# Kernel tuning notes

Hardware: AMD Instinct MI355X
Metric: run time of the kernel (lower is better)

The kernel has to match this reference:

```python
import jax, jax.numpy as jnp
import numpy as np


def setup_inputs() -> dict:
    key = jax.random.key(0)
    k1, k2, k3, k4 = jax.random.split(key, 4)
    B, C, H, W = 4, 512, 64, 64
    K = 20
    Cp = C // 4  # 128, proj_feat output channels
    feat = jax.random.normal(k1, (B, C, H, W), dtype=jnp.float32)
    cam = jax.random.uniform(k2, (B, K, H, W), dtype=jnp.float32)
    # 1x1 conv == linear over channel dim; store kernel as [Cout, Cin]
    w_proj = jax.random.normal(k3, (Cp, C), dtype=jnp.float32) * (1.0 / np.sqrt(C))
    b_proj = jax.random.normal(k4, (Cp,), dtype=jnp.float32) * 0.01
    return {"feat": feat, "cam": cam, "w_proj": w_proj, "b_proj": b_proj}


def reference(feat, cam, w_proj, b_proj):
    B, C, H, W = feat.shape
    K = cam.shape[1]
    N = H * W
    cam_detach = jax.lax.stop_gradient(cam)
    # proj_feat: 1x1 conv -> [B, N, C//4] token layout (matches view+transpose)
    feat_proj = jnp.einsum('bchw,oc->bhwo', feat, w_proj) + b_proj
    feat_proj = feat_proj.reshape(B, N, -1)                      # [B, N, Cp]
    cam_reshape = cam_detach.reshape(B, K, N)                    # [B, K, N]
    class_term = jnp.einsum('bkn,bnd->bkd', cam_reshape, feat_proj)  # [B, K, Cp]
    # unscaled self-attention over N pixels
    pixel_sim = jnp.einsum('bnd,bmd->bnm', feat_proj, feat_proj)     # [B, N, N]
    pixel_sim = jax.nn.softmax(pixel_sim, axis=-1)
    pixel_term = jnp.einsum('bnm,bmd->bnd', pixel_sim, feat_proj)    # [B, N, Cp]
    aug_cam = jnp.einsum('bkd,bnd->bkn', class_term, pixel_term)     # [B, K, N]
    return cam + aug_cam.reshape(B, K, H, W)
```

## Files before the change

kernel.cpp:

```cpp
#include <hip/hip_runtime.h>
#include <hip/hip_bf16.h>
#include <math.h>

#define NB 4
#define NC 512
#define NN 4096
#define NK 20
#define NCP 128
#define SPLIT 4
#define CHUNK (NN / SPLIT)
#define NTILES (CHUNK / 64)

typedef __bf16 bf16x8 __attribute__((ext_vector_type(8)));
typedef float f32x4 __attribute__((ext_vector_type(4)));
typedef float f32x16 __attribute__((ext_vector_type(16)));
typedef short short8 __attribute__((ext_vector_type(8)));
typedef unsigned int uint4v __attribute__((ext_vector_type(4)));

static __device__ __forceinline__ unsigned short f2bf(float f) {
    unsigned int u = __builtin_bit_cast(unsigned int, f);
    unsigned int r = (u + 0x7FFFu + ((u >> 16) & 1u)) >> 16;
    return (unsigned short)r;
}
static __device__ __forceinline__ float bf2f(unsigned short h) {
    unsigned int u = ((unsigned int)h) << 16;
    return __builtin_bit_cast(float, u);
}
static __device__ __forceinline__ bf16x8 ldbf8(const unsigned short* p) {
    return __builtin_bit_cast(bf16x8, *reinterpret_cast<const short8*>(p));
}
static __device__ __forceinline__ void gld16(const unsigned short* g, unsigned short* l) {
    __builtin_amdgcn_global_load_lds(
        (const __attribute__((address_space(1))) unsigned int*)g,
        (__attribute__((address_space(3))) unsigned int*)l, 16, 0, 0);
}
static __device__ __forceinline__ unsigned int cvtpk(float lo, float hi) {
    unsigned int r;
    asm("v_cvt_pk_bf16_f32 %0, %1, %2" : "=v"(r) : "v"(lo), "v"(hi));
    return r;
}

#define MFMA16(a, b, c) __builtin_amdgcn_mfma_f32_16x16x32_bf16(a, b, c, 0, 0, 0)
#define MFMA32(a, b, c) __builtin_amdgcn_mfma_f32_32x32x16_bf16(a, b, c, 0, 0, 0)
#define SCHED0() __builtin_amdgcn_sched_barrier(0)
#define BAR() do { SCHED0(); __builtin_amdgcn_s_barrier(); SCHED0(); } while (0)

__global__ __launch_bounds__(256) void wconv_kernel(
    const float* __restrict__ w, unsigned short* __restrict__ wb)
{
    int i = blockIdx.x * 256 + threadIdx.x;
    float4 v = reinterpret_cast<const float4*>(w)[i];
    unsigned int lo = (unsigned int)f2bf(v.x) | ((unsigned int)f2bf(v.y) << 16);
    unsigned int hi = (unsigned int)f2bf(v.z) | ((unsigned int)f2bf(v.w) << 16);
    reinterpret_cast<uint2*>(wb)[i] = make_uint2(lo, hi);
}

__global__ __launch_bounds__(256) void proj_kernel(
    const float* __restrict__ feat, const unsigned short* __restrict__ wb,
    const float* __restrict__ bias, unsigned short* __restrict__ fp,
    unsigned short* __restrict__ fpT)
{
    const int b = blockIdx.y;
    const int n0 = blockIdx.x * 64;
    const int tid = threadIdx.x;
    const int wid = tid >> 6;
    const int lane = tid & 63;
    const int lg = lane >> 4, lr = lane & 15;

    __shared__ unsigned short lds_f[2][64][40];

    const float* featb = feat + (size_t)b * NC * NN;

    f32x4 acc[2][4];
    #pragma unroll
    for (int i = 0; i < 2; ++i)
        #pragma unroll
        for (int j = 0; j < 4; ++j) acc[i][j] = (f32x4){0.f, 0.f, 0.f, 0.f};

    float4 pre[2];
    #pragma unroll
    for (int it = 0; it < 2; ++it) {
        int idx = it * 256 + tid;
        int cc = idx >> 4, q = idx & 15;
        pre[it] = *reinterpret_cast<const float4*>(&featb[(size_t)cc * NN + n0 + q * 4]);
    }

    for (int c0 = 0; c0 < NC; c0 += 32) {
        const int cur = (c0 >> 5) & 1;
        #pragma unroll
        for (int it = 0; it < 2; ++it) {
            int idx = it * 256 + tid;
            int cc = idx >> 4, q = idx & 15;
            float4 v = pre[it];
            lds_f[cur][q * 4 + 0][cc] = f2bf(v.x);
            lds_f[cur][q * 4 + 1][cc] = f2bf(v.y);
            lds_f[cur][q * 4 + 2][cc] = f2bf(v.z);
            lds_f[cur][q * 4 + 3][cc] = f2bf(v.w);
        }
        __syncthreads();
        if (c0 + 32 < NC) {
            #pragma unroll
            for (int it = 0; it < 2; ++it) {
                int idx = it * 256 + tid;
                int cc = idx >> 4, q = idx & 15;
                pre[it] = *reinterpret_cast<const float4*>(
                    &featb[(size_t)(c0 + 32 + cc) * NN + n0 + q * 4]);
            }
        }
        bf16x8 afr[2];
        #pragma unroll
        for (int dt = 0; dt < 2; ++dt)
            afr[dt] = ldbf8(&wb[(size_t)(wid * 32 + dt * 16 + lr) * NC + c0 + lg * 8]);
        #pragma unroll
        for (int n1 = 0; n1 < 4; ++n1) {
            bf16x8 bfr = ldbf8(&lds_f[cur][n1 * 16 + lr][lg * 8]);
            #pragma unroll
            for (int dt = 0; dt < 2; ++dt)
                acc[dt][n1] = MFMA16(afr[dt], bfr, acc[dt][n1]);
        }
    }
    #pragma unroll
    for (int dt = 0; dt < 2; ++dt)
        #pragma unroll
        for (int n1 = 0; n1 < 4; ++n1)
            #pragma unroll
            for (int i = 0; i < 4; ++i) {
                int d = wid * 32 + dt * 16 + lg * 4 + i;
                int n = n0 + n1 * 16 + lr;
                unsigned short h = f2bf(acc[dt][n1][i] + bias[d]);
                fp[((size_t)b * NN + n) * NCP + d] = h;
                fpT[((size_t)b * NCP + d) * NN + n] = h;
            }
}

__global__ __launch_bounds__(128) void ct_kernel(
    const float* __restrict__ cam, const unsigned short* __restrict__ fp,
    float* __restrict__ ct)
{
    const int bid = blockIdx.x;
    const int chunk = bid & 15;
    const int bk = bid >> 4;
    const int b = bk / NK, k = bk % NK;
    const int d2 = threadIdx.x & 63;
    const int half = threadIdx.x >> 6;
    const int nbase = chunk * 256 + half * 128;
    const float* camp = cam + ((size_t)b * NK + k) * NN + nbase;
    const unsigned short* fpp = fp + ((size_t)b * NN + nbase) * NCP + d2 * 2;
    float ax = 0.f, ay = 0.f;
    #pragma unroll 8
    for (int n = 0; n < 128; ++n) {
        float c = camp[n];
        unsigned int v = *reinterpret_cast<const unsigned int*>(&fpp[(size_t)n * NCP]);
        ax += c * bf2f((unsigned short)(v & 0xffff));
        ay += c * bf2f((unsigned short)(v >> 16));
    }
    float* ctp = &ct[((size_t)b * NK + k) * NCP + d2 * 2];
    atomicAdd(ctp, ax);
    atomicAdd(ctp + 1, ay);
}

__global__ __launch_bounds__(256, 3) void attn_partial_kernel(
    const unsigned short* __restrict__ fp, const unsigned short* __restrict__ fpT,
    unsigned short* __restrict__ po, float* __restrict__ mbuf, float* __restrict__ lbuf)
{
    const int b = blockIdx.z;
    const int sidx = blockIdx.y;
    const int tid = threadIdx.x;
    const int wid = tid >> 6;
    const int lane = tid & 63;
    const int l31 = lane & 31, hi = lane >> 5;
    const int q0 = blockIdx.x * 128 + wid * 32;
    const int kvbase = sidx * CHUNK;

    __shared__ unsigned short kt[2][64 * 128];
    __shared__ unsigned short vt[64 * 128];

    const unsigned short* fpb  = fp  + (size_t)b * NN * NCP;
    const unsigned short* fpTb = fpT + (size_t)b * NCP * NN;

    int offK[4], offV[4];
    #pragma unroll
    for (int i = 0; i < 4; ++i) {
        int oc = i * 256 + tid;
        int rk = oc >> 4, ck = oc & 15;
        offK[i] = rk * NCP + ((ck ^ (rk & 15)) << 3);
        int rowp = oc >> 4, cv = oc & 15;
        int cg = cv ^ (rowp & 15);
        int d = rowp * 2 + (cg >> 3), kvc = cg & 7;
        offV[i] = d * NN + (kvc << 3);
    }

    bf16x8 qf[8];
    #pragma unroll
    for (int kk = 0; kk < 8; ++kk)
        qf[kk] = ldbf8(&fpb[(size_t)(q0 + l31) * NCP + kk * 16 + hi * 8]);

    f32x16 o[4];
    #pragma unroll
    for (int dt = 0; dt < 4; ++dt)
        #pragma unroll
        for (int j = 0; j < 16; ++j) o[dt][j] = 0.f;
    float m_i = -INFINITY, l_i = 0.f;

    {
        const unsigned short* k0 = fpb + (size_t)kvbase * NCP;
        #pragma unroll
        for (int i = 0; i < 4; ++i)
            gld16(k0 + offK[i], &kt[0][(i * 256 + wid * 64) * 8]);
    }
    SCHED0();
    asm volatile("s_waitcnt vmcnt(0)" ::: "memory");
    BAR();

    for (int t = 0; t < NTILES; ++t) {
        const int cur = t & 1;
        {
            const unsigned short* vnow = fpTb + kvbase + t * 64;
            #pragma unroll
            for (int i = 0; i < 4; ++i)
                gld16(vnow + offV[i], &vt[(i * 256 + wid * 64) * 8]);
            const int tn = (t + 1) & (NTILES - 1);
            const unsigned short* knext = fpb + (size_t)(kvbase + tn * 64) * NCP;
            #pragma unroll
            for (int i = 0; i < 4; ++i)
                gld16(knext + offK[i], &kt[cur ^ 1][(i * 256 + wid * 64) * 8]);
        }
        SCHED0();
        const unsigned short* ktc = &kt[cur][0];
        f32x16 s[2];
        #pragma unroll
        for (int g = 0; g < 2; ++g)
            #pragma unroll
            for (int j = 0; j < 16; ++j) s[g][j] = 0.f;
        __builtin_amdgcn_s_setprio(1);
        #pragma unroll
        for (int kk = 0; kk < 8; ++kk) {
            #pragma unroll
            for (int g = 0; g < 2; ++g) {
                int row = g * 32 + l31;
                bf16x8 kf = ldbf8(&ktc[row * 128 + (((kk * 2 + hi) ^ (row & 15)) << 3)]);
                s[g] = MFMA32(kf, qf[kk], s[g]);
            }
        }
        __builtin_amdgcn_s_setprio(0);
        float pmax = s[0][0];
        #pragma unroll
        for (int g = 0; g < 2; ++g)
            #pragma unroll
            for (int j = 0; j < 16; ++j) pmax = fmaxf(pmax, s[g][j]);
        pmax = fmaxf(pmax, __shfl_xor(pmax, 32));
        if (!__all(pmax - m_i <= 8.f)) {
            float mnew = fmaxf(m_i, pmax);
            float sc = __expf(m_i - mnew);
            l_i *= sc;
            #pragma unroll
            for (int dt = 0; dt < 4; ++dt)
                #pragma unroll
                for (int j = 0; j < 16; ++j) o[dt][j] *= sc;
            m_i = mnew;
        }
        float sum = 0.f;
        #pragma unroll
        for (int g = 0; g < 2; ++g)
            #pragma unroll
            for (int j = 0; j < 16; ++j) {
                float e = __expf(s[g][j] - m_i);
                s[g][j] = e;
                sum += e;
            }
        sum += __shfl_xor(sum, 32);
        l_i += sum;
        unsigned int wk[2][8];
        #pragma unroll
        for (int g = 0; g < 2; ++g)
            #pragma unroll
            for (int m = 0; m < 8; ++m)
                wk[g][m] = cvtpk(s[g][2 * m], s[g][2 * m + 1]);
        bf16x8 pf[4];
        #pragma unroll
        for (int g = 0; g < 2; ++g)
            #pragma unroll
            for (int sub = 0; sub < 2; ++sub) {
                unsigned int A0 = wk[g][4 * sub],     B0 = wk[g][4 * sub + 2];
                unsigned int A1 = wk[g][4 * sub + 1], B1 = wk[g][4 * sub + 3];
                asm("v_permlane32_swap_b32 %0, %1" : "+v"(A0), "+v"(B0));
                asm("v_permlane32_swap_b32 %0, %1" : "+v"(A1), "+v"(B1));
                uint4v u;
                u[0] = A0; u[1] = A1; u[2] = B0; u[3] = B1;
                pf[2 * g + sub] = __builtin_bit_cast(bf16x8, u);
            }
        SCHED0();
        asm volatile("s_waitcnt vmcnt(4)" ::: "memory");
        BAR();
        __builtin_amdgcn_s_setprio(1);
        #pragma unroll
        for (int c2 = 0; c2 < 4; ++c2) {
            #pragma unroll
            for (int dt = 0; dt < 4; ++dt) {
                int row32 = dt * 32 + l31;
                int rowp = row32 >> 1;
                int chunk = (row32 & 1) * 8 + c2 * 2 + hi;
                bf16x8 vf = ldbf8(&vt[rowp * 128 + ((chunk ^ (rowp & 15)) << 3)]);
                o[dt] = MFMA32(vf, pf[c2], o[dt]);
            }
        }
        __builtin_amdgcn_s_setprio(0);
        SCHED0();
        asm volatile("s_waitcnt vmcnt(0)" ::: "memory");
        BAR();
    }
    const size_t pbase = (size_t)(b * SPLIT + sidx) * NN + q0;
    const size_t rowoff = (pbase + l31) * NCP;
    #pragma unroll
    for (int dt = 0; dt < 4; ++dt)
        #pragma unroll
        for (int qd = 0; qd < 4; ++qd) {
            unsigned int u0 = cvtpk(o[dt][qd * 4 + 0], o[dt][qd * 4 + 1]);
            unsigned int u1 = cvtpk(o[dt][qd * 4 + 2], o[dt][qd * 4 + 3]);
            *reinterpret_cast<uint2*>(&po[rowoff + dt * 32 + qd * 8 + hi * 4]) =
                make_uint2(u0, u1);
        }
    if (hi == 0) {
        mbuf[pbase + l31] = m_i;
        lbuf[pbase + l31] = l_i;
    }
}

__global__ __launch_bounds__(256) void aug_kernel(
    const float* __restrict__ cam, const float* __restrict__ ct,
    const unsigned short* __restrict__ po, const float* __restrict__ mbuf,
    const float* __restrict__ lbuf, float* __restrict__ out)
{
    const int b = blockIdx.y;
    const int tid = threadIdx.x, wid = tid >> 6, lane = tid & 63;
    const int lg = lane >> 4, lr = lane & 15;
    const int n0 = blockIdx.x * 64 + wid * 16;
    const int row = n0 + lr;
    const float* ctb = ct + (size_t)b * NK * NCP;

    float m_s[SPLIT], l_s[SPLIT], M = -INFINITY;
    #pragma unroll
    for (int s = 0; s < SPLIT; ++s) {
        m_s[s] = mbuf[(size_t)(b * SPLIT + s) * NN + row];
        l_s[s] = lbuf[(size_t)(b * SPLIT + s) * NN + row];
        M = fmaxf(M, m_s[s]);
    }
    float L = 0.f, wgt[SPLIT];
    #pragma unroll
    for (int s = 0; s < SPLIT; ++s) { wgt[s] = __expf(m_s[s] - M); L += wgt[s] * l_s[s]; }
    const float inv = 1.f / L;
    #pragma unroll
    for (int s = 0; s < SPLIT; ++s) wgt[s] *= inv;

    f32x4 acc[2];
    acc[0] = (f32x4){0.f, 0.f, 0.f, 0.f};
    acc[1] = (f32x4){0.f, 0.f, 0.f, 0.f};
    #pragma unroll
    for (int kk = 0; kk < 4; ++kk) {
        float mg[8];
        #pragma unroll
        for (int j = 0; j < 8; ++j) mg[j] = 0.f;
        #pragma unroll
        for (int s = 0; s < SPLIT; ++s) {
            uint4v v = *reinterpret_cast<const uint4v*>(
                &po[((size_t)(b * SPLIT + s) * NN + row) * NCP + kk * 32 + lg * 8]);
            #pragma unroll
            for (int j = 0; j < 4; ++j) {
                mg[2 * j]     += wgt[s] * bf2f((unsigned short)(v[j] & 0xffff));
                mg[2 * j + 1] += wgt[s] * bf2f((unsigned short)(v[j] >> 16));
            }
        }
        uint4v au;
        #pragma unroll
        for (int j = 0; j < 4; ++j) au[j] = cvtpk(mg[2 * j], mg[2 * j + 1]);
        bf16x8 af = __builtin_bit_cast(bf16x8, au);
        #pragma unroll
        for (int c = 0; c < 2; ++c) {
            int k = c * 16 + lr;
            short8 bv;
            if (k < NK) {
                const float* cr = &ctb[(size_t)k * NCP + kk * 32 + lg * 8];
                #pragma unroll
                for (int j = 0; j < 8; ++j) bv[j] = (short)f2bf(cr[j]);
            } else {
                #pragma unroll
                for (int j = 0; j < 8; ++j) bv[j] = 0;
            }
            acc[c] = MFMA16(af, __builtin_bit_cast(bf16x8, bv), acc[c]);
        }
    }
    #pragma unroll
    for (int c = 0; c < 2; ++c) {
        int k = c * 16 + lr;
        if (k < NK) {
            #pragma unroll
            for (int i = 0; i < 4; ++i) {
                size_t off = ((size_t)b * NK + k) * NN + n0 + lg * 4 + i;
                out[off] = cam[off] + acc[c][i];
            }
        }
    }
}

extern "C" void kernel_launch(void* const* d_in, const int* in_sizes, int n_in,
                              void* d_out, int out_size, void* d_ws, size_t ws_size,
                              hipStream_t stream) {
    const float* feat = (const float*)d_in[0];
    const float* cam  = (const float*)d_in[1];
    const float* wpr  = (const float*)d_in[2];
    const float* bpr  = (const float*)d_in[3];
    float* out = (float*)d_out;

    const size_t MB = 1024 * 1024;
    char* ws = (char*)d_ws;
    unsigned short* fp  = (unsigned short*)(ws);
    unsigned short* fpT = (unsigned short*)(ws + 4 * MB);
    float* ct           = (float*)(ws + 12 * MB);
    unsigned short* wb  = (unsigned short*)(ws + 12 * MB + 512 * 1024);
    unsigned short* po  = (unsigned short*)(ws + 13 * MB);
    float* mbuf         = (float*)(ws + 30 * MB);
    float* lbuf         = (float*)(ws + 31 * MB);

    hipMemsetAsync(ct, 0, (size_t)NB * NK * NCP * sizeof(float), stream);
    wconv_kernel<<<64, 256, 0, stream>>>(wpr, wb);
    proj_kernel<<<dim3(NN / 64, NB), 256, 0, stream>>>(feat, wb, bpr, fp, fpT);
    ct_kernel<<<NB * NK * 16, 128, 0, stream>>>(cam, fp, ct);
    attn_partial_kernel<<<dim3(NN / 128, SPLIT, NB), 256, 0, stream>>>(fp, fpT, po, mbuf, lbuf);
    aug_kernel<<<dim3(NN / 64, NB), 256, 0, stream>>>(cam, ct, po, mbuf, lbuf, out);
}
```

Measured before the change: 95.23 us.

## Double-buffer K and V tiles with smaller KV blocks and finer split

Shrinks the KV tile from 64 to 32 keys, double-buffers V alongside K so both are prefetched one tile ahead, and removes the mid-loop barrier. It also doubles the split-KV factor to 8 and raises the occupancy hint to 4 blocks per CU, which lowers LDS use per block and increases the number of blocks. The cost is more partial outputs to merge in the aug kernel (more workspace traffic) and fewer MFMAs per barrier, so there are more rescale and softmax passes per unit of work.

Result: slower. 125.8 us (+32.1%).

```diff
diff --git a/kernel.cpp b/kernel.cpp
--- a/kernel.cpp
+++ b/kernel.cpp
@@ -7,9 +7,10 @@
 #define NN 4096
 #define NK 20
 #define NCP 128
-#define SPLIT 4
+#define SPLIT 8
 #define CHUNK (NN / SPLIT)
-#define NTILES (CHUNK / 64)
+#define KVB 32
+#define NTILES (CHUNK / KVB)
 
 typedef __bf16 bf16x8 __attribute__((ext_vector_type(8)));
 typedef float f32x4 __attribute__((ext_vector_type(4)));
@@ -159,7 +160,7 @@
     atomicAdd(ctp + 1, ay);
 }
 
-__global__ __launch_bounds__(256, 3) void attn_partial_kernel(
+__global__ __launch_bounds__(256, 4) void attn_partial_kernel(
     const unsigned short* __restrict__ fp, const unsigned short* __restrict__ fpT,
     unsigned short* __restrict__ po, float* __restrict__ mbuf, float* __restrict__ lbuf)
 {
@@ -172,21 +173,21 @@
     const int q0 = blockIdx.x * 128 + wid * 32;
     const int kvbase = sidx * CHUNK;
 
-    __shared__ unsigned short kt[2][64 * 128];
-    __shared__ unsigned short vt[64 * 128];
+    __shared__ unsigned short kt[2][KVB * 128];
+    __shared__ unsigned short vt[2][64 * 64];
 
     const unsigned short* fpb  = fp  + (size_t)b * NN * NCP;
     const unsigned short* fpTb = fpT + (size_t)b * NCP * NN;
 
-    int offK[4], offV[4];
-    #pragma unroll
-    for (int i = 0; i < 4; ++i) {
+    int offK[2], offV[2];
+    #pragma unroll
+    for (int i = 0; i < 2; ++i) {
         int oc = i * 256 + tid;
         int rk = oc >> 4, ck = oc & 15;
         offK[i] = rk * NCP + ((ck ^ (rk & 15)) << 3);
-        int rowp = oc >> 4, cv = oc & 15;
-        int cg = cv ^ (rowp & 15);
-        int d = rowp * 2 + (cg >> 3), kvc = cg & 7;
+        int rowp = oc >> 3, cv = oc & 7;
+        int cg = cv ^ (rowp & 7);
+        int d = rowp * 2 + (cg >> 2), kvc = cg & 3;
         offV[i] = d * NN + (kvc << 3);
     }
 
@@ -204,9 +205,12 @@
 
     {
         const unsigned short* k0 = fpb + (size_t)kvbase * NCP;
-        #pragma unroll
-        for (int i = 0; i < 4; ++i)
+        const unsigned short* v0 = fpTb + kvbase;
+        #pragma unroll
+        for (int i = 0; i < 2; ++i) {
             gld16(k0 + offK[i], &kt[0][(i * 256 + wid * 64) * 8]);
+            gld16(v0 + offV[i], &vt[0][(i * 256 + wid * 64) * 8]);
+        }
     }
     SCHED0();
     asm volatile("s_waitcnt vmcnt(0)" ::: "memory");
@@ -214,40 +218,30 @@
 
     for (int t = 0; t < NTILES; ++t) {
         const int cur = t & 1;
-        {
-            const unsigned short* vnow = fpTb + kvbase + t * 64;
-            #pragma unroll
-            for (int i = 0; i < 4; ++i)
-                gld16(vnow + offV[i], &vt[(i * 256 + wid * 64) * 8]);
-            const int tn = (t + 1) & (NTILES - 1);
-            const unsigned short* knext = fpb + (size_t)(kvbase + tn * 64) * NCP;
-            #pragma unroll
-            for (int i = 0; i < 4; ++i)
+        if (t + 1 < NTILES) {
+            const unsigned short* knext = fpb + (size_t)(kvbase + (t + 1) * KVB) * NCP;
+            const unsigned short* vnext = fpTb + kvbase + (t + 1) * KVB;
+            #pragma unroll
+            for (int i = 0; i < 2; ++i) {
                 gld16(knext + offK[i], &kt[cur ^ 1][(i * 256 + wid * 64) * 8]);
+                gld16(vnext + offV[i], &vt[cur ^ 1][(i * 256 + wid * 64) * 8]);
+            }
         }
         SCHED0();
         const unsigned short* ktc = &kt[cur][0];
-        f32x16 s[2];
-        #pragma unroll
-        for (int g = 0; g < 2; ++g)
-            #pragma unroll
-            for (int j = 0; j < 16; ++j) s[g][j] = 0.f;
+        f32x16 s;
+        #pragma unroll
+        for (int j = 0; j < 16; ++j) s[j] = 0.f;
         __builtin_amdgcn_s_setprio(1);
         #pragma unroll
         for (int kk = 0; kk < 8; ++kk) {
-            #pragma unroll
-            for (int g = 0; g < 2; ++g) {
-                int row = g * 32 + l31;
-                bf16x8 kf = ldbf8(&ktc[row * 128 + (((kk * 2 + hi) ^ (row & 15)) << 3)]);
-                s[g] = MFMA32(kf, qf[kk], s[g]);
-            }
+            bf16x8 kf = ldbf8(&ktc[l31 * 128 + (((kk * 2 + hi) ^ (l31 & 15)) << 3)]);
+            s = MFMA32(kf, qf[kk], s);
         }
         __builtin_amdgcn_s_setprio(0);
-        float pmax = s[0][0];
-        #pragma unroll
-        for (int g = 0; g < 2; ++g)
-            #pragma unroll
-            for (int j = 0; j < 16; ++j) pmax = fmaxf(pmax, s[g][j]);
+        float pmax = s[0];
+        #pragma unroll
+        for (int j = 1; j < 16; ++j) pmax = fmaxf(pmax, s[j]);
         pmax = fmaxf(pmax, __shfl_xor(pmax, 32));
         if (!__all(pmax - m_i <= 8.f)) {
             float mnew = fmaxf(m_i, pmax);
@@ -261,46 +255,38 @@
         }
         float sum = 0.f;
         #pragma unroll
-        for (int g = 0; g < 2; ++g)
-            #pragma unroll
-            for (int j = 0; j < 16; ++j) {
-                float e = __expf(s[g][j] - m_i);
-                s[g][j] = e;
-                sum += e;
-            }
+        for (int j = 0; j < 16; ++j) {
+            float e = __expf(s[j] - m_i);
+            s[j] = e;
+            sum += e;
+        }
         sum += __shfl_xor(sum, 32);
         l_i += sum;
-        unsigned int wk[2][8];
-        #pragma unroll
-        for (int g = 0; g < 2; ++g)
-            #pragma unroll
-            for (int m = 0; m < 8; ++m)
-                wk[g][m] = cvtpk(s[g][2 * m], s[g][2 * m + 1]);
-        bf16x8 pf[4];
-        #pragma unroll
-        for (int g = 0; g < 2; ++g)
-            #pragma unroll
-            for (int sub = 0; sub < 2; ++sub) {
-                unsigned int A0 = wk[g][4 * sub],     B0 = wk[g][4 * sub + 2];
-                unsigned int A1 = wk[g][4 * sub + 1], B1 = wk[g][4 * sub + 3];
-                asm("v_permlane32_swap_b32 %0, %1" : "+v"(A0), "+v"(B0));
-                asm("v_permlane32_swap_b32 %0, %1" : "+v"(A1), "+v"(B1));
-                uint4v u;
-                u[0] = A0; u[1] = A1; u[2] = B0; u[3] = B1;
-                pf[2 * g + sub] = __builtin_bit_cast(bf16x8, u);
-            }
-        SCHED0();
-        asm volatile("s_waitcnt vmcnt(4)" ::: "memory");
-        BAR();
+        unsigned int wk[8];
+        #pragma unroll
+        for (int m = 0; m < 8; ++m)
+            wk[m] = cvtpk(s[2 * m], s[2 * m + 1]);
+        bf16x8 pf[2];
+        #pragma unroll
+        for (int sub = 0; sub < 2; ++sub) {
+            unsigned int A0 = wk[4 * sub],     B0 = wk[4 * sub + 2];
+            unsigned int A1 = wk[4 * sub + 1], B1 = wk[4 * sub + 3];
+            asm("v_permlane32_swap_b32 %0, %1" : "+v"(A0), "+v"(B0));
+            asm("v_permlane32_swap_b32 %0, %1" : "+v"(A1), "+v"(B1));
+            uint4v u;
+            u[0] = A0; u[1] = A1; u[2] = B0; u[3] = B1;
+            pf[sub] = __builtin_bit_cast(bf16x8, u);
+        }
+        const unsigned short* vtc = &vt[cur][0];
         __builtin_amdgcn_s_setprio(1);
         #pragma unroll
-        for (int c2 = 0; c2 < 4; ++c2) {
+        for (int c2 = 0; c2 < 2; ++c2) {
             #pragma unroll
             for (int dt = 0; dt < 4; ++dt) {
                 int row32 = dt * 32 + l31;
                 int rowp = row32 >> 1;
-                int chunk = (row32 & 1) * 8 + c2 * 2 + hi;
-                bf16x8 vf = ldbf8(&vt[rowp * 128 + ((chunk ^ (rowp & 15)) << 3)]);
+                int chunk = (row32 & 1) * 4 + c2 * 2 + hi;
+                bf16x8 vf = ldbf8(&vtc[rowp * 64 + ((chunk ^ (rowp & 7)) << 3)]);
                 o[dt] = MFMA32(vf, pf[c2], o[dt]);
             }
         }
@@ -418,8 +404,8 @@
     float* ct           = (float*)(ws + 12 * MB);
     unsigned short* wb  = (unsigned short*)(ws + 12 * MB + 512 * 1024);
     unsigned short* po  = (unsigned short*)(ws + 13 * MB);
-    float* mbuf         = (float*)(ws + 30 * MB);
-    float* lbuf         = (float*)(ws + 31 * MB);
+    float* mbuf         = (float*)(ws + 45 * MB);
+    float* lbuf         = (float*)(ws + 46 * MB);
 
     hipMemsetAsync(ct, 0, (size_t)NB * NK * NCP * sizeof(float), stream);
     wconv_kernel<<<64, 256, 0, stream>>>(wpr, wb);
```

## Double-buffer V tiles in attention and fuse weight conversion into projection

Applied to the files above, without the earlier changes.

The attention kernel now double-buffers the V tile alongside K. The next tile's K and V are prefetched together, which removes the mid-iteration wait and barrier before the PV MFMAs. This raises LDS use to 64KB per block, so launch bounds drop from 3 to 2 blocks per SM. Separately, the weight-to-bf16 conversion kernel is removed and proj_kernel converts fp32 weights inline, saving a launch at the cost of extra fp32 loads and redundant conversion work across blocks.

Measured after the change: 94.96 us. No clear change (-0.3%).

```diff
diff --git a/kernel.cpp b/kernel.cpp
--- a/kernel.cpp
+++ b/kernel.cpp
@@ -45,18 +45,8 @@
 #define SCHED0() __builtin_amdgcn_sched_barrier(0)
 #define BAR() do { SCHED0(); __builtin_amdgcn_s_barrier(); SCHED0(); } while (0)
 
-__global__ __launch_bounds__(256) void wconv_kernel(
-    const float* __restrict__ w, unsigned short* __restrict__ wb)
-{
-    int i = blockIdx.x * 256 + threadIdx.x;
-    float4 v = reinterpret_cast<const float4*>(w)[i];
-    unsigned int lo = (unsigned int)f2bf(v.x) | ((unsigned int)f2bf(v.y) << 16);
-    unsigned int hi = (unsigned int)f2bf(v.z) | ((unsigned int)f2bf(v.w) << 16);
-    reinterpret_cast<uint2*>(wb)[i] = make_uint2(lo, hi);
-}
-
 __global__ __launch_bounds__(256) void proj_kernel(
-    const float* __restrict__ feat, const unsigned short* __restrict__ wb,
+    const float* __restrict__ feat, const float* __restrict__ w,
     const float* __restrict__ bias, unsigned short* __restrict__ fp,
     unsigned short* __restrict__ fpT)
 {
@@ -109,8 +99,17 @@
         }
         bf16x8 afr[2];
         #pragma unroll
-        for (int dt = 0; dt < 2; ++dt)
-            afr[dt] = ldbf8(&wb[(size_t)(wid * 32 + dt * 16 + lr) * NC + c0 + lg * 8]);
+        for (int dt = 0; dt < 2; ++dt) {
+            const float4* wr = reinterpret_cast<const float4*>(
+                w + (size_t)(wid * 32 + dt * 16 + lr) * NC + c0 + lg * 8);
+            float4 w0 = wr[0], w1 = wr[1];
+            short8 a;
+            a[0] = (short)f2bf(w0.x); a[1] = (short)f2bf(w0.y);
+            a[2] = (short)f2bf(w0.z); a[3] = (short)f2bf(w0.w);
+            a[4] = (short)f2bf(w1.x); a[5] = (short)f2bf(w1.y);
+            a[6] = (short)f2bf(w1.z); a[7] = (short)f2bf(w1.w);
+            afr[dt] = __builtin_bit_cast(bf16x8, a);
+        }
         #pragma unroll
         for (int n1 = 0; n1 < 4; ++n1) {
             bf16x8 bfr = ldbf8(&lds_f[cur][n1 * 16 + lr][lg * 8]);
@@ -159,7 +158,7 @@
     atomicAdd(ctp + 1, ay);
 }
 
-__global__ __launch_bounds__(256, 3) void attn_partial_kernel(
+__global__ __launch_bounds__(256, 2) void attn_partial_kernel(
     const unsigned short* __restrict__ fp, const unsigned short* __restrict__ fpT,
     unsigned short* __restrict__ po, float* __restrict__ mbuf, float* __restrict__ lbuf)
 {
@@ -173,7 +172,7 @@
     const int kvbase = sidx * CHUNK;
 
     __shared__ unsigned short kt[2][64 * 128];
-    __shared__ unsigned short vt[64 * 128];
+    __shared__ unsigned short vt[2][64 * 128];
 
     const unsigned short* fpb  = fp  + (size_t)b * NN * NCP;
     const unsigned short* fpTb = fpT + (size_t)b * NCP * NN;
@@ -204,9 +203,12 @@
 
     {
         const unsigned short* k0 = fpb + (size_t)kvbase * NCP;
-        #pragma unroll
-        for (int i = 0; i < 4; ++i)
+        const unsigned short* v0 = fpTb + kvbase;
+        #pragma unroll
+        for (int i = 0; i < 4; ++i) {
             gld16(k0 + offK[i], &kt[0][(i * 256 + wid * 64) * 8]);
+            gld16(v0 + offV[i], &vt[0][(i * 256 + wid * 64) * 8]);
+        }
     }
     SCHED0();
     asm volatile("s_waitcnt vmcnt(0)" ::: "memory");
@@ -215,15 +217,14 @@
     for (int t = 0; t < NTILES; ++t) {
         const int cur = t & 1;
         {
-            const unsigned short* vnow = fpTb + kvbase + t * 64;
-            #pragma unroll
-            for (int i = 0; i < 4; ++i)
-                gld16(vnow + offV[i], &vt[(i * 256 + wid * 64) * 8]);
             const int tn = (t + 1) & (NTILES - 1);
             const unsigned short* knext = fpb + (size_t)(kvbase + tn * 64) * NCP;
-            #pragma unroll
-            for (int i = 0; i < 4; ++i)
+            const unsigned short* vnext = fpTb + kvbase + tn * 64;
+            #pragma unroll
+            for (int i = 0; i < 4; ++i) {
                 gld16(knext + offK[i], &kt[cur ^ 1][(i * 256 + wid * 64) * 8]);
+                gld16(vnext + offV[i], &vt[cur ^ 1][(i * 256 + wid * 64) * 8]);
+            }
         }
         SCHED0();
         const unsigned short* ktc = &kt[cur][0];
@@ -289,9 +290,7 @@
                 u[0] = A0; u[1] = A1; u[2] = B0; u[3] = B1;
                 pf[2 * g + sub] = __builtin_bit_cast(bf16x8, u);
             }
-        SCHED0();
-        asm volatile("s_waitcnt vmcnt(4)" ::: "memory");
-        BAR();
+        const unsigned short* vtc = &vt[cur][0];
         __builtin_amdgcn_s_setprio(1);
         #pragma unroll
         for (int c2 = 0; c2 < 4; ++c2) {
@@ -300,7 +299,7 @@
                 int row32 = dt * 32 + l31;
                 int rowp = row32 >> 1;
                 int chunk = (row32 & 1) * 8 + c2 * 2 + hi;
-                bf16x8 vf = ldbf8(&vt[rowp * 128 + ((chunk ^ (rowp & 15)) << 3)]);
+                bf16x8 vf = ldbf8(&vtc[rowp * 128 + ((chunk ^ (rowp & 15)) << 3)]);
                 o[dt] = MFMA32(vf, pf[c2], o[dt]);
             }
         }
@@ -416,14 +415,12 @@
     unsigned short* fp  = (unsigned short*)(ws);
     unsigned short* fpT = (unsigned short*)(ws + 4 * MB);
     float* ct           = (float*)(ws + 12 * MB);
-    unsigned short* wb  = (unsigned short*)(ws + 12 * MB + 512 * 1024);
     unsigned short* po  = (unsigned short*)(ws + 13 * MB);
     float* mbuf         = (float*)(ws + 30 * MB);
     float* lbuf         = (float*)(ws + 31 * MB);
 
     hipMemsetAsync(ct, 0, (size_t)NB * NK * NCP * sizeof(float), stream);
-    wconv_kernel<<<64, 256, 0, stream>>>(wpr, wb);
-    proj_kernel<<<dim3(NN / 64, NB), 256, 0, stream>>>(feat, wb, bpr, fp, fpT);
+    proj_kernel<<<dim3(NN / 64, NB), 256, 0, stream>>>(feat, wpr, bpr, fp, fpT);
     ct_kernel<<<NB * NK * 16, 128, 0, stream>>>(cam, fp, ct);
     attn_partial_kernel<<<dim3(NN / 128, SPLIT, NB), 256, 0, stream>>>(fp, fpT, po, mbuf, lbuf);
     aug_kernel<<<dim3(NN / 64, NB), 256, 0, stream>>>(cam, ct, po, mbuf, lbuf, out);
```
